# Optimization experiments

Hardware: AMD Instinct MI355X
Metric: run time of the kernel (lower is better)

Reference implementation:

```python
import jax, jax.numpy as jnp
import numpy as np
from jax import lax

DN = ('NCHW', 'OIHW', 'NCHW')
KD, VD, C = 32, 128, 256
NCLS, HW_T = 20, 32
LEVEL_SIZES = [128, 64, 32, 16, 8]
BS = 2


def conv2d(x, w, b):
    y = lax.conv_general_dilated(x, w, (1, 1), 'SAME', dimension_numbers=DN)
    return y + b[None, :, None, None]


def resize_bilinear_ac(x, oh, ow):
    # bilinear, align_corners=True, NCHW
    B, Cc, H, W = x.shape
    ys = jnp.linspace(0.0, H - 1.0, oh)
    xs = jnp.linspace(0.0, W - 1.0, ow)
    y0 = jnp.floor(ys).astype(jnp.int32); y1 = jnp.minimum(y0 + 1, H - 1)
    x0 = jnp.floor(xs).astype(jnp.int32); x1 = jnp.minimum(x0 + 1, W - 1)
    wy = (ys - y0).astype(x.dtype); wx = (xs - x0).astype(x.dtype)
    r0 = x[:, :, y0, :]; r1 = x[:, :, y1, :]
    rows = r0 + (r1 - r0) * wy[None, None, :, None]
    c0 = rows[:, :, :, x0]; c1 = rows[:, :, :, x1]
    return c0 + (c1 - c0) * wx[None, None, None, :]


def setup_inputs() -> dict:
    key = jax.random.key(0)
    ks = jax.random.split(key, 16)
    inp = {}
    for i, s in enumerate(LEVEL_SIZES):
        inp[f'feat{i}'] = jax.random.normal(ks[i], (BS, C, s, s), jnp.float32)
    inp['attentions'] = jax.random.normal(ks[5], (NCLS, C, HW_T, HW_T), jnp.float32)
    w = 0.05
    inp['key_t_w'] = jax.random.normal(ks[6], (KD, C, 3, 3), jnp.float32) * w
    inp['key_t_b'] = jax.random.normal(ks[7], (KD,), jnp.float32) * w
    inp['val_t_w'] = jax.random.normal(ks[8], (VD, C, 3, 3), jnp.float32) * w
    inp['val_t_b'] = jax.random.normal(ks[9], (VD,), jnp.float32) * w
    inp['key_q_w'] = jax.random.normal(ks[10], (5, KD, C, 3, 3), jnp.float32) * w
    inp['key_q_b'] = jax.random.normal(ks[11], (5, KD), jnp.float32) * w
    inp['val_q_w'] = jax.random.normal(ks[12], (5, VD, C, 3, 3), jnp.float32) * w
    inp['val_q_b'] = jax.random.normal(ks[13], (5, VD), jnp.float32) * w
    inp['bn_gamma'] = jnp.ones((5, C), jnp.float32)
    inp['bn_beta'] = jnp.zeros((5, C), jnp.float32)
    inp['comb_w'] = jax.random.normal(ks[14], (C, 2 * C, 1, 1), jnp.float32) * w
    inp['comb_b'] = jax.random.normal(ks[15], (C,), jnp.float32) * w
    return inp


def reference(feat0, feat1, feat2, feat3, feat4, attentions,
              key_t_w, key_t_b, val_t_w, val_t_b,
              key_q_w, key_q_b, val_q_w, val_q_b,
              bn_gamma, bn_beta, comb_w, comb_b):
    feats = [feat0, feat1, feat2, feat3, feat4]
    ncls, _, h, w = attentions.shape
    key_t = conv2d(attentions, key_t_w, key_t_b).reshape(ncls, KD, h * w)   # [n,32,t]
    val_t = conv2d(attentions, val_t_w, val_t_b).reshape(ncls, VD, h * w)   # [n,128,t]
    outs = []
    for idx, f in enumerate(feats):
        bs, _, H, W = f.shape
        fc = f - f.mean(axis=(2, 3), keepdims=True)          # subtract foregap
        fr = resize_bilinear_ac(fc, h, w)                    # [b,256,h,w]
        kq = conv2d(fr, key_q_w[idx], key_q_b[idx]).reshape(bs, KD, h * w)  # [b,32,q]
        vq = conv2d(fr, val_q_w[idx], val_q_b[idx]).reshape(bs, VD, h * w)  # [b,128,q]
        # relation: p[b,n,q,t] = kq^T @ key_t ; softmax over q (torch dim=1)
        p = jnp.einsum('bcq,nct->bnqt', kq, key_t)
        p = jax.nn.softmax(p, axis=2)
        # class-summed attended values (sum over n commutes with concat-add loop)
        vt_sum = jnp.einsum('nvq,bnqt->bvt', val_t, p)
        vq_sum = jnp.einsum('bvq,bnqt->bvt', vq, p)
        fin = jnp.concatenate([vq_sum, vt_sum], axis=1).reshape(bs, 2 * VD, h, w)
        fin = resize_bilinear_ac(fin, H, W)
        # BatchNorm2d (training-mode batch stats, eps=1e-5)
        mu = fin.mean(axis=(0, 2, 3), keepdims=True)
        var = fin.var(axis=(0, 2, 3), keepdims=True)
        fin = (fin - mu) * lax.rsqrt(var + 1e-5)
        fin = fin * bn_gamma[idx][None, :, None, None] + bn_beta[idx][None, :, None, None]
        out = conv2d(jnp.concatenate([f, fin], axis=1), comb_w, comb_b)
        outs.append(out)
    return tuple(outs)
```

## Files before the change

### kernel.cpp

```cpp
#include <hip/hip_runtime.h>
#include <cstddef>
#include <cstdint>

typedef __attribute__((ext_vector_type(8))) short bf16x8;
typedef __attribute__((ext_vector_type(16))) float f32x16;
typedef __attribute__((ext_vector_type(4))) unsigned short us4;

static const size_t B_BIASC = 0;
static const size_t B_KTH   = 3840;
static const size_t B_KTL   = 1314560;
static const size_t B_VT    = 2625280;
static const size_t B_KQH   = 7868160;
static const size_t B_KQL   = 8523520;
static const size_t B_VQ    = 9178880;
static const size_t B_MEAN  = 11800320;
static const size_t B_FSM   = 11810560;
static const size_t B_MU    = 17053440;
static const size_t B_VAR   = 17058560;
static const size_t B_WC    = 17063680;
static const size_t B_BIAS2 = 18374400;
static const size_t B_UNION = 18379520;
static const size_t U_XH    = 0;
static const size_t U_XL    = 15728640;
static const size_t U_WPH   = 31457280;
static const size_t U_WPL   = 35880960;
static const size_t U_FPART = 0;
static const size_t WS_BYTES = 58684160;

__device__ inline unsigned short f2bf(float x) {
    unsigned u = __float_as_uint(x);
    return (unsigned short)((u + 0x7fffu + ((u >> 16) & 1u)) >> 16);
}
__device__ inline float bf2f(unsigned short u) {
    return __uint_as_float(((unsigned)u) << 16);
}
__device__ inline void bf16split(float x, unsigned short& hi, unsigned short& lo) {
    unsigned u = __float_as_uint(x);
    unsigned hb = (u + 0x7fffu + ((u >> 16) & 1u)) >> 16;
    hi = (unsigned short)hb;
    float hf = __uint_as_float(hb << 16);
    float r = x - hf;
    unsigned ur = __float_as_uint(r);
    lo = (unsigned short)((ur + 0x7fffu + ((ur >> 16) & 1u)) >> 16);
}
__device__ inline const float* sel5(const float* a, const float* b, const float* c,
                                    const float* d, const float* e, int i) {
    return i == 0 ? a : i == 1 ? b : i == 2 ? c : i == 3 ? d : e;
}

__global__ __launch_bounds__(256) void prep_weights(
    const float* __restrict__ kt_w, const float* __restrict__ kt_b,
    const float* __restrict__ vt_w, const float* __restrict__ vt_b,
    const float* __restrict__ kq_w, const float* __restrict__ kq_b,
    const float* __restrict__ vq_w, const float* __restrict__ vq_b,
    short* __restrict__ wp_hi, short* __restrict__ wp_lo, float* __restrict__ biasc)
{
    const int oc = blockIdx.x;
    const int s  = blockIdx.y;
    const int ic = threadIdx.x;
    const bool iskey = oc < 32;
    const int ocl = iskey ? oc : oc - 32;
    const float scale = (iskey && s > 0) ? 1.4426950408889634f : 1.0f;
    const float* w = iskey
        ? (s == 0 ? kt_w : kq_w + (size_t)(s - 1) * 32 * 256 * 9)
        : (s == 0 ? vt_w : vq_w + (size_t)(s - 1) * 128 * 256 * 9);
    const float* wsrc = w + ((size_t)ocl * 256 + ic) * 9;
#pragma unroll
    for (int t = 0; t < 9; ++t) {
        unsigned short h, l; bf16split(wsrc[t] * scale, h, l);
        size_t d = ((size_t)(s * 9 + t) * 160 + oc) * 256 + ic;
        wp_hi[d] = (short)h; wp_lo[d] = (short)l;
    }
    if (ic == 0) {
        const float* bptr = iskey
            ? (s == 0 ? kt_b : kq_b + (s - 1) * 32)
            : (s == 0 ? vt_b : vq_b + (s - 1) * 128);
        biasc[s * 160 + oc] = bptr[ocl] * scale;
    }
}

__global__ __launch_bounds__(256) void transpose_split(
    const float* __restrict__ in,
    unsigned short* __restrict__ oh, unsigned short* __restrict__ ol)
{
    __shared__ float s[16][260];
    const int n = blockIdx.x, ch = blockIdx.y, p0 = blockIdx.z * 256;
    const int tid = threadIdx.x;
#pragma unroll
    for (int i = 0; i < 16; ++i)
        s[i][tid] = in[((size_t)(n * 256 + ch * 16 + i)) * 1024 + p0 + tid];
    __syncthreads();
    union { unsigned short u[16]; bf16x8 v[2]; } h8, l8;
#pragma unroll
    for (int i = 0; i < 16; ++i) bf16split(s[i][tid], h8.u[i], l8.u[i]);
    size_t base = ((size_t)(n * 16 + ch) * 1024 + p0 + tid) * 16;
    *(bf16x8*)&oh[base] = h8.v[0]; *(bf16x8*)&oh[base + 8] = h8.v[1];
    *(bf16x8*)&ol[base] = l8.v[0]; *(bf16x8*)&ol[base + 8] = l8.v[1];
}

__global__ __launch_bounds__(256) void mean2d_all(
    const float* f0, const float* f1, const float* f2, const float* f3, const float* f4,
    float* __restrict__ mean)
{
    const int lvl = blockIdx.y;
    const float* f = sel5(f0, f1, f2, f3, f4, lvl);
    const int H = 128 >> lvl, HW = H * H;
    const int bc = blockIdx.x;
    const float* src = f + (size_t)bc * HW;
    float s = 0.f;
    for (int i = threadIdx.x; i < HW; i += 256) s += src[i];
#pragma unroll
    for (int off = 32; off; off >>= 1) s += __shfl_xor(s, off);
    __shared__ float red[4];
    if ((threadIdx.x & 63) == 0) red[threadIdx.x >> 6] = s;
    __syncthreads();
    if (threadIdx.x == 0)
        mean[lvl * 512 + bc] = (red[0] + red[1] + red[2] + red[3]) / (float)HW;
}

__global__ __launch_bounds__(256) void resizeT_all(
    const float* f0, const float* f1, const float* f2, const float* f3, const float* f4,
    const float* __restrict__ mean,
    unsigned short* __restrict__ oh, unsigned short* __restrict__ ol)
{
    __shared__ float s[16][260];
    const int lvl = blockIdx.z >> 2;
    const int p0 = (blockIdx.z & 3) * 256;
    const int b = blockIdx.x, ch = blockIdx.y;
    const float* f = sel5(f0, f1, f2, f3, f4, lvl);
    const int H = 128 >> lvl;
    const int img = 20 + lvl * 2 + b;
    const int tid = threadIdx.x;
    const int p = p0 + tid, y = p >> 5, x = p & 31;
    float fy = (float)y * (float)(H - 1) / 31.0f;
    float fx = (float)x * (float)(H - 1) / 31.0f;
    int y0 = (int)fy; int y1 = min(y0 + 1, H - 1); float wy = fy - (float)y0;
    int x0 = (int)fx; int x1 = min(x0 + 1, H - 1); float wx = fx - (float)x0;
#pragma unroll
    for (int i = 0; i < 16; ++i) {
        int c = ch * 16 + i;
        const float* pf = f + ((size_t)(b * 256 + c)) * H * H;
        float a = pf[y0 * H + x0], bb = pf[y1 * H + x0];
        float cc = pf[y0 * H + x1], d = pf[y1 * H + x1];
        float c0 = a + (bb - a) * wy;
        float c1 = cc + (d - cc) * wy;
        s[i][tid] = c0 + (c1 - c0) * wx - mean[lvl * 512 + b * 256 + c];
    }
    __syncthreads();
    union { unsigned short u[16]; bf16x8 v[2]; } h8, l8;
#pragma unroll
    for (int i = 0; i < 16; ++i) bf16split(s[i][tid], h8.u[i], l8.u[i]);
    size_t base = ((size_t)(img * 16 + ch) * 1024 + p) * 16;
    *(bf16x8*)&oh[base] = h8.v[0]; *(bf16x8*)&oh[base + 8] = h8.v[1];
    *(bf16x8*)&ol[base] = l8.v[0]; *(bf16x8*)&ol[base + 8] = l8.v[1];
}

__global__ __launch_bounds__(256) void conv3x3_direct(
    const unsigned short* __restrict__ xT_h,
    const unsigned short* __restrict__ xT_l,
    const short* __restrict__ wp_hi_all,
    const short* __restrict__ wp_lo_all,
    const float* __restrict__ biasc_all,
    unsigned short* __restrict__ kt_hi, unsigned short* __restrict__ kt_lo,
    unsigned short* __restrict__ vt,
    unsigned short* __restrict__ kq_hi, unsigned short* __restrict__ kq_lo,
    unsigned short* __restrict__ vq)
{
    const int tid = threadIdx.x;
    const int img = blockIdx.x;
    const int grp = blockIdx.z;
    const bool iskey = (grp == 0);
    const int set = (img < 20) ? 0 : 1 + ((img - 20) >> 1);
    const int ocb = grp * 32;
    const int wave = tid >> 6, l31 = tid & 31, lh = (tid >> 5) & 1;
    const int yp = blockIdx.y * 4 + wave;
    const int y0 = yp * 2;

    f32x16 acc0 = {}, acc1 = {};
    const bf16x8 bz = {};
    const unsigned short* xh = xT_h + (size_t)img * 16 * 16384;
    const unsigned short* xl = xT_l + (size_t)img * 16 * 16384;
    const short* wph = wp_hi_all + (size_t)set * 368640;
    const short* wpl = wp_lo_all + (size_t)set * 368640;
    const float* bset = biasc_all + set * 160;

    for (int ch = 0; ch < 16; ++ch) {
        const unsigned short* xhc = xh + (size_t)ch * 16384 + lh * 8;
        const unsigned short* xlc = xl + (size_t)ch * 16384 + lh * 8;
#pragma unroll
        for (int tg = 0; tg < 3; ++tg) {
            bf16x8 wh[3], wl[3];
#pragma unroll
            for (int tl = 0; tl < 3; ++tl) {
                size_t wi = ((size_t)((tg * 3 + tl) * 160 + ocb + l31)) * 256 + (ch << 4) + lh * 8;
                wh[tl] = *(const bf16x8*)&wph[wi];
                if (iskey) wl[tl] = *(const bf16x8*)&wpl[wi];
            }
#pragma unroll
            for (int nt = 0; nt < 2; ++nt) {
                const int ri = y0 + nt - 1 + tg;
                const bool rok = (ri >= 0 && ri < 32);
#pragma unroll
                for (int tl = 0; tl < 3; ++tl) {
                    const int x = l31 + tl - 1;
                    const bool ok = rok && (x >= 0) && (x < 32);
                    bf16x8 bh = bz, bl = bz;
                    if (ok) {
                        const int p = ri * 32 + x;
                        bh = *(const bf16x8*)&xhc[p * 16];
                        if (iskey) bl = *(const bf16x8*)&xlc[p * 16];
                    }
                    f32x16& a = nt ? acc1 : acc0;
                    a = __builtin_amdgcn_mfma_f32_32x32x16_bf16(wh[tl], bh, a, 0, 0, 0);
                    if (iskey) {
                        a = __builtin_amdgcn_mfma_f32_32x32x16_bf16(wh[tl], bl, a, 0, 0, 0);
                        a = __builtin_amdgcn_mfma_f32_32x32x16_bf16(wl[tl], bh, a, 0, 0, 0);
                    }
                }
            }
        }
    }
    if (iskey) {
#pragma unroll
        for (int nt = 0; nt < 2; ++nt) {
            const f32x16& a = nt ? acc1 : acc0;
            int p = (y0 + nt) * 32 + l31;
            size_t base = (img < 20)
                ? ((size_t)img * 1024 + p) * 32
                : ((size_t)(img - 20) * 1024 + p) * 32;
            unsigned short* oh = (img < 20) ? kt_hi : kq_hi;
            unsigned short* ol = (img < 20) ? kt_lo : kq_lo;
#pragma unroll
            for (int qd = 0; qd < 4; ++qd) {
                int ocq = 8 * qd + 4 * lh;
                us4 h4, l4;
#pragma unroll
                for (int j = 0; j < 4; ++j) {
                    unsigned short h, l;
                    bf16split(a[qd * 4 + j] + bset[ocq + j], h, l);
                    h4[j] = h; l4[j] = l;
                }
                *(us4*)&oh[base + ocq] = h4;
                *(us4*)&ol[base + ocq] = l4;
            }
        }
    } else {
        unsigned short* ov = (img < 20) ? vt : vq;
        const int iml = (img < 20) ? img : img - 20;
#pragma unroll
        for (int nt = 0; nt < 2; ++nt) {
            const f32x16& a = nt ? acc1 : acc0;
            int p = (y0 + nt) * 32 + l31;
#pragma unroll
            for (int r = 0; r < 16; ++r) {
                int pat = (r & 3) + 8 * (r >> 2) + 4 * lh;
                int vo = (ocb - 32) + pat;
                ov[((size_t)iml * 128 + vo) * 1024 + p] = f2bf(a[r] + bset[ocb + pat]);
            }
        }
    }
}

__global__ __launch_bounds__(256, 3) void flash2(
    const unsigned short* __restrict__ kt_hi, const unsigned short* __restrict__ kt_lo,
    const unsigned short* __restrict__ vt_bf,
    const unsigned short* __restrict__ kq_hi, const unsigned short* __restrict__ kq_lo,
    const unsigned short* __restrict__ vq_bf,
    unsigned short* __restrict__ fin_part)
{
    __shared__ unsigned short s_v[256 * 40];
    const int tid = threadIdx.x;
    const int t0 = blockIdx.x * 64;
    const int b  = blockIdx.y;
    const int n  = blockIdx.z;
    const int wave = tid >> 6, lane = tid & 63, l31 = lane & 31, lh = lane >> 5;
    const int tw = wave & 1, vw = wave >> 1;

    const int trow = t0 + tw * 32 + l31;
    bf16x8 btk_h0, btk_h1, btk_l0, btk_l1;
    {
        size_t g = ((size_t)n * 1024 + trow) * 32 + lh * 8;
        btk_h0 = *(const bf16x8*)&kt_hi[g];
        btk_h1 = *(const bf16x8*)&kt_hi[g + 16];
        btk_l0 = *(const bf16x8*)&kt_lo[g];
        btk_l1 = *(const bf16x8*)&kt_lo[g + 16];
    }

    const unsigned short* vsrc = (tid < 128)
        ? &vq_bf[((size_t)b * 128 + tid) * 1024]
        : &vt_bf[((size_t)n * 128 + (tid - 128)) * 1024];
    const unsigned short* kqh = kq_hi + (size_t)b * 1024 * 32;
    const unsigned short* kql = kq_lo + (size_t)b * 1024 * 32;

    bf16x8 nv0 = *(const bf16x8*)&vsrc[0];
    bf16x8 nv1 = *(const bf16x8*)&vsrc[8];
    bf16x8 nv2 = *(const bf16x8*)&vsrc[16];
    bf16x8 nv3 = *(const bf16x8*)&vsrc[24];
    bf16x8 nah0 = *(const bf16x8*)&kqh[(size_t)l31 * 32 + lh * 8];
    bf16x8 nah1 = *(const bf16x8*)&kqh[(size_t)l31 * 32 + 16 + lh * 8];
    bf16x8 nal0 = *(const bf16x8*)&kql[(size_t)l31 * 32 + lh * 8];
    bf16x8 nal1 = *(const bf16x8*)&kql[(size_t)l31 * 32 + 16 + lh * 8];

    f32x16 acc0 = {}, acc1 = {}, acc2 = {}, acc3 = {};
    float m = -3.0e38f, lsum = 0.f;

    for (int q0 = 0; q0 < 1024; q0 += 32) {
        __syncthreads();
        {
            unsigned short* dst = &s_v[tid * 40];
            *(bf16x8*)&dst[0]  = nv0;
            *(bf16x8*)&dst[8]  = nv1;
            *(bf16x8*)&dst[16] = nv2;
            *(bf16x8*)&dst[24] = nv3;
        }
        bf16x8 ah0 = nah0, ah1 = nah1, al0 = nal0, al1 = nal1;
        __syncthreads();

        if (q0 + 32 < 1024) {
            const int qn = q0 + 32;
            nv0 = *(const bf16x8*)&vsrc[qn];
            nv1 = *(const bf16x8*)&vsrc[qn + 8];
            nv2 = *(const bf16x8*)&vsrc[qn + 16];
            nv3 = *(const bf16x8*)&vsrc[qn + 24];
            size_t kb = (size_t)(qn + l31) * 32 + lh * 8;
            nah0 = *(const bf16x8*)&kqh[kb];
            nah1 = *(const bf16x8*)&kqh[kb + 16];
            nal0 = *(const bf16x8*)&kql[kb];
            nal1 = *(const bf16x8*)&kql[kb + 16];
        }

        f32x16 s = {};
        s = __builtin_amdgcn_mfma_f32_32x32x16_bf16(ah0, btk_h0, s, 0, 0, 0);
        s = __builtin_amdgcn_mfma_f32_32x32x16_bf16(ah0, btk_l0, s, 0, 0, 0);
        s = __builtin_amdgcn_mfma_f32_32x32x16_bf16(al0, btk_h0, s, 0, 0, 0);
        s = __builtin_amdgcn_mfma_f32_32x32x16_bf16(ah1, btk_h1, s, 0, 0, 0);
        s = __builtin_amdgcn_mfma_f32_32x32x16_bf16(ah1, btk_l1, s, 0, 0, 0);
        s = __builtin_amdgcn_mfma_f32_32x32x16_bf16(al1, btk_h1, s, 0, 0, 0);

        float pmax = s[0];
#pragma unroll
        for (int r = 1; r < 16; ++r) pmax = fmaxf(pmax, s[r]);
        pmax = fmaxf(pmax, __shfl_xor(pmax, 32));
        if (!__all(pmax <= m + 11.5417f)) {
            float mnew = fmaxf(m, pmax);
            float sc = __builtin_amdgcn_exp2f(m - mnew);
            m = mnew; lsum *= sc;
            acc0 *= sc; acc1 *= sc; acc2 *= sc; acc3 *= sc;
        }
        float pv[16]; float ps = 0.f;
#pragma unroll
        for (int r = 0; r < 16; ++r) { pv[r] = __builtin_amdgcn_exp2f(s[r] - m); ps += pv[r]; }
        lsum += ps;

        unsigned a0, a1, a2, a3, c0, c1, c2, c3;
        asm("v_cvt_pk_bf16_f32 %0, %1, %2" : "=v"(a0) : "v"(pv[0]),  "v"(pv[1]));
        asm("v_cvt_pk_bf16_f32 %0, %1, %2" : "=v"(a1) : "v"(pv[2]),  "v"(pv[3]));
        asm("v_cvt_pk_bf16_f32 %0, %1, %2" : "=v"(a2) : "v"(pv[4]),  "v"(pv[5]));
        asm("v_cvt_pk_bf16_f32 %0, %1, %2" : "=v"(a3) : "v"(pv[6]),  "v"(pv[7]));
        asm("v_cvt_pk_bf16_f32 %0, %1, %2" : "=v"(c0) : "v"(pv[8]),  "v"(pv[9]));
        asm("v_cvt_pk_bf16_f32 %0, %1, %2" : "=v"(c1) : "v"(pv[10]), "v"(pv[11]));
        asm("v_cvt_pk_bf16_f32 %0, %1, %2" : "=v"(c2) : "v"(pv[12]), "v"(pv[13]));
        asm("v_cvt_pk_bf16_f32 %0, %1, %2" : "=v"(c3) : "v"(pv[14]), "v"(pv[15]));
        asm("v_permlane32_swap_b32 %0, %1" : "+v"(a0), "+v"(a2));
        asm("v_permlane32_swap_b32 %0, %1" : "+v"(a1), "+v"(a3));
        asm("v_permlane32_swap_b32 %0, %1" : "+v"(c0), "+v"(c2));
        asm("v_permlane32_swap_b32 %0, %1" : "+v"(c1), "+v"(c3));
        union { unsigned u[4]; bf16x8 v; } f0, f1;
        f0.u[0] = a0; f0.u[1] = a1; f0.u[2] = a2; f0.u[3] = a3;
        f1.u[0] = c0; f1.u[1] = c1; f1.u[2] = c2; f1.u[3] = c3;

#pragma unroll
        for (int vs = 0; vs < 4; ++vs) {
            const unsigned short* vr = &s_v[(vw * 128 + vs * 32 + l31) * 40 + lh * 8];
            bf16x8 va0 = *(const bf16x8*)&vr[0];
            bf16x8 va1 = *(const bf16x8*)&vr[16];
            f32x16& a = (vs == 0) ? acc0 : (vs == 1) ? acc1 : (vs == 2) ? acc2 : acc3;
            a = __builtin_amdgcn_mfma_f32_32x32x16_bf16(va0, f0.v, a, 0, 0, 0);
            a = __builtin_amdgcn_mfma_f32_32x32x16_bf16(va1, f1.v, a, 0, 0, 0);
        }
    }

    float lt = lsum + __shfl_xor(lsum, 32);
    float linv = 1.f / lt;
    unsigned short* outp = fin_part + ((size_t)(n * 2 + b)) * 256 * 1024;
    const int tg = t0 + tw * 32 + l31;
#pragma unroll
    for (int vs = 0; vs < 4; ++vs) {
        const f32x16& a = (vs == 0) ? acc0 : (vs == 1) ? acc1 : (vs == 2) ? acc2 : acc3;
#pragma unroll
        for (int r = 0; r < 16; ++r) {
            int v = vw * 128 + vs * 32 + (r & 3) + 8 * (r >> 2) + 4 * lh;
            outp[(size_t)v * 1024 + tg] = f2bf(a[r] * linv);
        }
    }
}

__global__ __launch_bounds__(256) void reduce20_bf(
    const unsigned short* __restrict__ part, unsigned short* __restrict__ out)
{
    size_t i = (size_t)blockIdx.x * 256 + threadIdx.x;
    float s = 0.f;
#pragma unroll
    for (int nn = 0; nn < 20; ++nn) s += bf2f(part[(size_t)nn * 524288 + i]);
    out[i] = f2bf(s);
}

__global__ __launch_bounds__(256) void upsample_bf(
    const unsigned short* __restrict__ in,
    float* __restrict__ out,
    int oh, int ow, int total)
{
    int idx = blockIdx.x * 256 + threadIdx.x;
    if (idx >= total) return;
    int x  = idx % ow;
    int y  = (idx / ow) % oh;
    int bc = idx / (ow * oh);
    float fy = (float)y * 31.0f / (float)(oh - 1);
    float fx = (float)x * 31.0f / (float)(ow - 1);
    int y0 = (int)fy; int y1 = min(y0 + 1, 31); float wy = fy - (float)y0;
    int x0 = (int)fx; int x1 = min(x0 + 1, 31); float wx = fx - (float)x0;
    const unsigned short* p = in + (size_t)bc * 1024;
    float a = bf2f(p[y0 * 32 + x0]), b = bf2f(p[y1 * 32 + x0]);
    float c = bf2f(p[y0 * 32 + x1]), d = bf2f(p[y1 * 32 + x1]);
    float c0 = a + (b - a) * wy;
    float c1 = c + (d - c) * wy;
    out[idx] = c0 + (c1 - c0) * wx;
}

__global__ __launch_bounds__(256) void bnstats_kernel(
    const float* __restrict__ fin, float* __restrict__ mu, float* __restrict__ var, int HW)
{
    const int c = blockIdx.x;
    float s = 0.f, s2 = 0.f;
    for (int b = 0; b < 2; ++b) {
        const float* p = fin + ((size_t)b * 256 + c) * HW;
        for (int i = threadIdx.x; i < HW; i += 256) {
            float v = p[i]; s += v; s2 += v * v;
        }
    }
#pragma unroll
    for (int off = 32; off; off >>= 1) {
        s  += __shfl_xor(s, off);
        s2 += __shfl_xor(s2, off);
    }
    __shared__ float r1[4], r2[4];
    if ((threadIdx.x & 63) == 0) { r1[threadIdx.x >> 6] = s; r2[threadIdx.x >> 6] = s2; }
    __syncthreads();
    if (threadIdx.x == 0) {
        float cnt = 2.f * (float)HW;
        float mm = (r1[0] + r1[1] + r1[2] + r1[3]) / cnt;
        float qq = (r2[0] + r2[1] + r2[2] + r2[3]) / cnt;
        mu[c] = mm; var[c] = qq - mm * mm;
    }
}

__global__ __launch_bounds__(256) void prep_comb(
    const float* __restrict__ comb_w, const float* __restrict__ comb_b,
    const float* __restrict__ gamma, const float* __restrict__ beta,
    const float* __restrict__ mu, const float* __restrict__ var,
    short* __restrict__ wc, float* __restrict__ bias2)
{
    const int oc = blockIdx.x;
    const int ic = threadIdx.x;
    float a  = gamma[ic] * rsqrtf(var[ic] + 1e-5f);
    float bb = beta[ic] - mu[ic] * a;
    float w1 = comb_w[(size_t)oc * 512 + ic];
    float w2 = comb_w[(size_t)oc * 512 + 256 + ic];
    wc[(size_t)oc * 512 + ic]       = (short)f2bf(w1);
    wc[(size_t)oc * 512 + 256 + ic] = (short)f2bf(w2 * a);
    float s = w2 * bb;
#pragma unroll
    for (int off = 32; off; off >>= 1) s += __shfl_xor(s, off);
    __shared__ float red[4];
    if ((threadIdx.x & 63) == 0) red[threadIdx.x >> 6] = s;
    __syncthreads();
    if (threadIdx.x == 0)
        bias2[oc] = comb_b[oc] + red[0] + red[1] + red[2] + red[3];
}

__global__ __launch_bounds__(256, 1) void comb_mfma(
    const float* __restrict__ f,
    const float* __restrict__ fin,
    const short* __restrict__ wc,
    const float* __restrict__ bias2,
    float* __restrict__ out, int HW)
{
    __shared__ short s_wc[256 * 40];
    __shared__ short s_xc[128 * 40];
    const int tid = threadIdx.x;
    const int p0 = blockIdx.x * 128;
    const int b  = blockIdx.y;
    const int wv = tid >> 6, l31 = tid & 31, lh = (tid >> 5) & 1;
    const int wm = wv >> 1, wn = wv & 1;

    f32x16 acc[4][2];
#pragma unroll
    for (int i = 0; i < 4; ++i)
#pragma unroll
        for (int j = 0; j < 2; ++j)
#pragma unroll
            for (int r = 0; r < 16; ++r) acc[i][j][r] = 0.f;

    for (int k0 = 0; k0 < 512; k0 += 32) {
        __syncthreads();
        for (int u = tid; u < 512; u += 256) {
            int r = u >> 1, h = u & 1;
            *(bf16x8*)&s_wc[r * 40 + h * 16 + 0] = *(const bf16x8*)&wc[(size_t)r * 512 + k0 + h * 16];
            *(bf16x8*)&s_wc[r * 40 + h * 16 + 8] = *(const bf16x8*)&wc[(size_t)r * 512 + k0 + h * 16 + 8];
        }
        for (int u = tid; u < 1024; u += 256) {
            int kr = u >> 5, n4 = (u & 31) * 4;
            int ck = k0 + kr;
            const float* bsrc = (ck < 256)
                ? f   + ((size_t)(b * 256 + ck)) * HW
                : fin + ((size_t)(b * 256 + ck - 256)) * HW;
            int p = p0 + n4;
            float v0, v1, v2, v3;
            if (p + 3 < HW) {
                float4 v4 = *(const float4*)&bsrc[p];
                v0 = v4.x; v1 = v4.y; v2 = v4.z; v3 = v4.w;
            } else {
                v0 = bsrc[min(p,     HW - 1)];
                v1 = bsrc[min(p + 1, HW - 1)];
                v2 = bsrc[min(p + 2, HW - 1)];
                v3 = bsrc[min(p + 3, HW - 1)];
            }
            s_xc[(n4 + 0) * 40 + kr] = (short)f2bf(v0);
            s_xc[(n4 + 1) * 40 + kr] = (short)f2bf(v1);
            s_xc[(n4 + 2) * 40 + kr] = (short)f2bf(v2);
            s_xc[(n4 + 3) * 40 + kr] = (short)f2bf(v3);
        }
        __syncthreads();
#pragma unroll
        for (int ks = 0; ks < 2; ++ks) {
            bf16x8 a[4], bx[2];
#pragma unroll
            for (int mi = 0; mi < 4; ++mi)
                a[mi] = *(const bf16x8*)&s_wc[(wm * 128 + mi * 32 + l31) * 40 + ks * 16 + lh * 8];
#pragma unroll
            for (int ni = 0; ni < 2; ++ni)
                bx[ni] = *(const bf16x8*)&s_xc[(wn * 64 + ni * 32 + l31) * 40 + ks * 16 + lh * 8];
#pragma unroll
            for (int mi = 0; mi < 4; ++mi)
#pragma unroll
                for (int ni = 0; ni < 2; ++ni)
                    acc[mi][ni] = __builtin_amdgcn_mfma_f32_32x32x16_bf16(a[mi], bx[ni], acc[mi][ni], 0, 0, 0);
        }
    }
#pragma unroll
    for (int mi = 0; mi < 4; ++mi) {
#pragma unroll
        for (int ni = 0; ni < 2; ++ni) {
            int p = p0 + wn * 64 + ni * 32 + l31;
            if (p < HW) {
#pragma unroll
                for (int r = 0; r < 16; ++r) {
                    int oc = wm * 128 + mi * 32 + (r & 3) + 8 * (r >> 2) + 4 * lh;
                    out[((size_t)(b * 256 + oc)) * HW + p] = acc[mi][ni][r] + bias2[oc];
                }
            }
        }
    }
}

extern "C" void kernel_launch(void* const* d_in, const int* in_sizes, int n_in,
                              void* d_out, int out_size, void* d_ws, size_t ws_size,
                              hipStream_t stream) {
    if (ws_size < WS_BYTES) return;

    const float* feats[5];
    for (int i = 0; i < 5; ++i) feats[i] = (const float*)d_in[i];
    const float* attn     = (const float*)d_in[5];
    const float* key_t_w  = (const float*)d_in[6];
    const float* key_t_b  = (const float*)d_in[7];
    const float* val_t_w  = (const float*)d_in[8];
    const float* val_t_b  = (const float*)d_in[9];
    const float* key_q_w  = (const float*)d_in[10];
    const float* key_q_b  = (const float*)d_in[11];
    const float* val_q_w  = (const float*)d_in[12];
    const float* val_q_b  = (const float*)d_in[13];
    const float* bn_gamma = (const float*)d_in[14];
    const float* bn_beta  = (const float*)d_in[15];
    const float* comb_w   = (const float*)d_in[16];
    const float* comb_b   = (const float*)d_in[17];

    char* ws = (char*)d_ws;
    float* biasc = (float*)(ws + B_BIASC);
    unsigned short* kt_hi = (unsigned short*)(ws + B_KTH);
    unsigned short* kt_lo = (unsigned short*)(ws + B_KTL);
    unsigned short* vt    = (unsigned short*)(ws + B_VT);
    unsigned short* kq_hi = (unsigned short*)(ws + B_KQH);
    unsigned short* kq_lo = (unsigned short*)(ws + B_KQL);
    unsigned short* vq    = (unsigned short*)(ws + B_VQ);
    float* mean_f = (float*)(ws + B_MEAN);
    unsigned short* fsm = (unsigned short*)(ws + B_FSM);
    float* mu     = (float*)(ws + B_MU);
    float* var    = (float*)(ws + B_VAR);
    short* wc_bf  = (short*)(ws + B_WC);
    float* bias2  = (float*)(ws + B_BIAS2);
    unsigned short* X_h = (unsigned short*)(ws + B_UNION + U_XH);
    unsigned short* X_l = (unsigned short*)(ws + B_UNION + U_XL);
    short* wp_hi = (short*)(ws + B_UNION + U_WPH);
    short* wp_lo = (short*)(ws + B_UNION + U_WPL);
    unsigned short* fin_part = (unsigned short*)(ws + B_UNION + U_FPART);
    float* fin_big = (float*)(ws + B_UNION);

    prep_weights<<<dim3(160, 6), 256, 0, stream>>>(
        key_t_w, key_t_b, val_t_w, val_t_b, key_q_w, key_q_b, val_q_w, val_q_b,
        wp_hi, wp_lo, biasc);

    transpose_split<<<dim3(20, 16, 4), 256, 0, stream>>>(attn, X_h, X_l);

    mean2d_all<<<dim3(512, 5), 256, 0, stream>>>(
        feats[0], feats[1], feats[2], feats[3], feats[4], mean_f);

    resizeT_all<<<dim3(2, 16, 20), 256, 0, stream>>>(
        feats[0], feats[1], feats[2], feats[3], feats[4], mean_f, X_h, X_l);

    conv3x3_direct<<<dim3(30, 4, 5), 256, 0, stream>>>(
        X_h, X_l, wp_hi, wp_lo, biasc, kt_hi, kt_lo, vt, kq_hi, kq_lo, vq);

    size_t out_off = 0;
    for (int idx = 0; idx < 5; ++idx) {
        const int H = 128 >> idx, HW = H * H;
        const int total = 2 * 256 * HW;

        flash2<<<dim3(16, 2, 20), 256, 0, stream>>>(
            kt_hi, kt_lo, vt,
            kq_hi + (size_t)idx * 2 * 32768,
            kq_lo + (size_t)idx * 2 * 32768,
            vq + (size_t)idx * 2 * 131072,
            fin_part);

        reduce20_bf<<<2048, 256, 0, stream>>>(fin_part, fsm + (size_t)idx * 524288);

        upsample_bf<<<(total + 255) / 256, 256, 0, stream>>>(
            fsm + (size_t)idx * 524288, fin_big, H, H, total);

        bnstats_kernel<<<256, 256, 0, stream>>>(fin_big, mu + idx * 256, var + idx * 256, HW);

        prep_comb<<<256, 256, 0, stream>>>(
            comb_w, comb_b, bn_gamma + idx * 256, bn_beta + idx * 256,
            mu + idx * 256, var + idx * 256, wc_bf + (size_t)idx * 131072, bias2 + idx * 256);

        comb_mfma<<<dim3((HW + 127) / 128, 2), 256, 0, stream>>>(
            feats[idx], fin_big, wc_bf + (size_t)idx * 131072, bias2 + idx * 256,
            (float*)d_out + out_off, HW);

        out_off += (size_t)2 * 256 * HW;
    }
}
```

Baseline: 921.6 us.

## Split conv channel loop across waves with LDS reduction; double-buffer flash2 V tile

Measured after the change: 893.9 us. 3.0% less time.

```diff
diff --git a/kernel.cpp b/kernel.cpp
--- a/kernel.cpp
+++ b/kernel.cpp
@@ -155,7 +155,7 @@
     *(bf16x8*)&ol[base] = l8.v[0]; *(bf16x8*)&ol[base + 8] = l8.v[1];
 }
 
-__global__ __launch_bounds__(256) void conv3x3_direct(
+__global__ __launch_bounds__(256) void conv3x3_all(
     const unsigned short* __restrict__ xT_h,
     const unsigned short* __restrict__ xT_l,
     const short* __restrict__ wp_hi_all,
@@ -166,14 +166,15 @@
     unsigned short* __restrict__ kq_hi, unsigned short* __restrict__ kq_lo,
     unsigned short* __restrict__ vq)
 {
+    __shared__ float s_red[4][2][16][64];
     const int tid = threadIdx.x;
     const int img = blockIdx.x;
+    const int yp  = blockIdx.y;
     const int grp = blockIdx.z;
     const bool iskey = (grp == 0);
     const int set = (img < 20) ? 0 : 1 + ((img - 20) >> 1);
     const int ocb = grp * 32;
-    const int wave = tid >> 6, l31 = tid & 31, lh = (tid >> 5) & 1;
-    const int yp = blockIdx.y * 4 + wave;
+    const int wave = tid >> 6, lane = tid & 63, l31 = tid & 31, lh = (tid >> 5) & 1;
     const int y0 = yp * 2;
 
     f32x16 acc0 = {}, acc1 = {};
@@ -184,7 +185,8 @@
     const short* wpl = wp_lo_all + (size_t)set * 368640;
     const float* bset = biasc_all + set * 160;
 
-    for (int ch = 0; ch < 16; ++ch) {
+    for (int cc = 0; cc < 4; ++cc) {
+        const int ch = (wave << 2) + cc;
         const unsigned short* xhc = xh + (size_t)ch * 16384 + lh * 8;
         const unsigned short* xlc = xl + (size_t)ch * 16384 + lh * 8;
 #pragma unroll
@@ -220,42 +222,54 @@
             }
         }
     }
+#pragma unroll
+    for (int r = 0; r < 16; ++r) {
+        s_red[wave][0][r][lane] = acc0[r];
+        s_red[wave][1][r][lane] = acc1[r];
+    }
+    __syncthreads();
+    float r0[4], r1[4];
+#pragma unroll
+    for (int j = 0; j < 4; ++j) {
+        int r = (wave << 2) + j;
+        r0[j] = s_red[0][0][r][lane] + s_red[1][0][r][lane] + s_red[2][0][r][lane] + s_red[3][0][r][lane];
+        r1[j] = s_red[0][1][r][lane] + s_red[1][1][r][lane] + s_red[2][1][r][lane] + s_red[3][1][r][lane];
+    }
     if (iskey) {
 #pragma unroll
         for (int nt = 0; nt < 2; ++nt) {
-            const f32x16& a = nt ? acc1 : acc0;
+            const float* rr = nt ? r1 : r0;
             int p = (y0 + nt) * 32 + l31;
-            size_t base = (img < 20)
-                ? ((size_t)img * 1024 + p) * 32
-                : ((size_t)(img - 20) * 1024 + p) * 32;
-            unsigned short* oh = (img < 20) ? kt_hi : kq_hi;
-            unsigned short* ol = (img < 20) ? kt_lo : kq_lo;
-#pragma unroll
-            for (int qd = 0; qd < 4; ++qd) {
-                int ocq = 8 * qd + 4 * lh;
-                us4 h4, l4;
-#pragma unroll
-                for (int j = 0; j < 4; ++j) {
-                    unsigned short h, l;
-                    bf16split(a[qd * 4 + j] + bset[ocq + j], h, l);
-                    h4[j] = h; l4[j] = l;
-                }
-                *(us4*)&oh[base + ocq] = h4;
-                *(us4*)&ol[base + ocq] = l4;
+            int ocq = 8 * wave + 4 * lh;
+            us4 h4, l4;
+#pragma unroll
+            for (int j = 0; j < 4; ++j) {
+                unsigned short h, l;
+                bf16split(rr[j] + bset[ocq + j], h, l);
+                h4[j] = h; l4[j] = l;
             }
+            if (img < 20) {
+                size_t base = ((size_t)img * 1024 + p) * 32;
+                *(us4*)&kt_hi[base + ocq] = h4;
+                *(us4*)&kt_lo[base + ocq] = l4;
+            } else {
+                size_t base = ((size_t)(img - 20) * 1024 + p) * 32;
+                *(us4*)&kq_hi[base + ocq] = h4;
+                *(us4*)&kq_lo[base + ocq] = l4;
+            }
         }
     } else {
-        unsigned short* ov = (img < 20) ? vt : vq;
-        const int iml = (img < 20) ? img : img - 20;
 #pragma unroll
         for (int nt = 0; nt < 2; ++nt) {
-            const f32x16& a = nt ? acc1 : acc0;
+            const float* rr = nt ? r1 : r0;
             int p = (y0 + nt) * 32 + l31;
 #pragma unroll
-            for (int r = 0; r < 16; ++r) {
-                int pat = (r & 3) + 8 * (r >> 2) + 4 * lh;
+            for (int j = 0; j < 4; ++j) {
+                int pat = j + 8 * wave + 4 * lh;
                 int vo = (ocb - 32) + pat;
-                ov[((size_t)iml * 128 + vo) * 1024 + p] = f2bf(a[r] + bset[ocb + pat]);
+                unsigned short val = f2bf(rr[j] + bset[32 + vo]);
+                if (img < 20) vt[((size_t)img * 128 + vo) * 1024 + p] = val;
+                else          vq[((size_t)(img - 20) * 128 + vo) * 1024 + p] = val;
             }
         }
     }
@@ -268,7 +282,7 @@
     const unsigned short* __restrict__ vq_bf,
     unsigned short* __restrict__ fin_part)
 {
-    __shared__ unsigned short s_v[256 * 40];
+    __shared__ unsigned short s_v[2][256 * 40];
     const int tid = threadIdx.x;
     const int t0 = blockIdx.x * 64;
     const int b  = blockIdx.y;
@@ -305,16 +319,15 @@
     float m = -3.0e38f, lsum = 0.f;
 
     for (int q0 = 0; q0 < 1024; q0 += 32) {
-        __syncthreads();
+        const int c = (q0 >> 5) & 1;
         {
-            unsigned short* dst = &s_v[tid * 40];
+            unsigned short* dst = &s_v[c][tid * 40];
             *(bf16x8*)&dst[0]  = nv0;
             *(bf16x8*)&dst[8]  = nv1;
             *(bf16x8*)&dst[16] = nv2;
             *(bf16x8*)&dst[24] = nv3;
         }
         bf16x8 ah0 = nah0, ah1 = nah1, al0 = nal0, al1 = nal1;
-        __syncthreads();
 
         if (q0 + 32 < 1024) {
             const int qn = q0 + 32;
@@ -328,6 +341,7 @@
             nal0 = *(const bf16x8*)&kql[kb];
             nal1 = *(const bf16x8*)&kql[kb + 16];
         }
+        __syncthreads();
 
         f32x16 s = {};
         s = __builtin_amdgcn_mfma_f32_32x32x16_bf16(ah0, btk_h0, s, 0, 0, 0);
@@ -371,7 +385,7 @@
 
 #pragma unroll
         for (int vs = 0; vs < 4; ++vs) {
-            const unsigned short* vr = &s_v[(vw * 128 + vs * 32 + l31) * 40 + lh * 8];
+            const unsigned short* vr = &s_v[c][(vw * 128 + vs * 32 + l31) * 40 + lh * 8];
             bf16x8 va0 = *(const bf16x8*)&vr[0];
             bf16x8 va1 = *(const bf16x8*)&vr[16];
             f32x16& a = (vs == 0) ? acc0 : (vs == 1) ? acc1 : (vs == 2) ? acc2 : acc3;
@@ -617,7 +631,7 @@
     resizeT_all<<<dim3(2, 16, 20), 256, 0, stream>>>(
         feats[0], feats[1], feats[2], feats[3], feats[4], mean_f, X_h, X_l);
 
-    conv3x3_direct<<<dim3(30, 4, 5), 256, 0, stream>>>(
+    conv3x3_all<<<dim3(30, 16, 5), 256, 0, stream>>>(
         X_h, X_l, wp_hi, wp_lo, biasc, kt_hi, kt_lo, vt, kq_hi, kq_lo, vq);
 
     size_t out_off = 0;
```
